# Kernel tuning notes

Measured on AMD Instinct MI355X. Metric: run time of the kernel, lower is better.

The kernel has to match this reference:

```python
import jax, jax.numpy as jnp
import numpy as np
import math

D_MODEL = 512
N_HEADS = 8
MAX_SPAN = 512
SPAN_LOSS_COEF = 2e-4
NEG_INF = -1.0e9
R_SIZE = 4.0


def soft_span_mask(span, max_span, seq_len):
    # span: (H,) clamped span fractions
    i_idx = jnp.arange(seq_len, dtype=span.dtype)[:, None]
    j_idx = jnp.arange(seq_len, dtype=span.dtype)[None, :]
    dist = i_idx - j_idx                                  # (T, T)
    eff_span = (span * max_span)[:, None, None]           # (H, 1, 1)
    x = eff_span - dist[None, :, :]                       # (H, T, T)
    R = jnp.clip((x + 1.0) / R_SIZE, 0.0, 1.0)
    causal_ok = dist[None, :, :] >= 0
    log_R = jnp.maximum(jnp.log(R + 1e-10), NEG_INF)
    return jnp.where(causal_ok & (R > 0), log_R, NEG_INF)  # (H, T, T)


def setup_inputs() -> dict:
    key = jax.random.key(0)
    ks = jax.random.split(key, 6)
    B, T, D = 4, 2048, D_MODEL
    w_scale = 0.02
    return {
        "x": jax.random.normal(ks[0], (B, T, D), dtype=jnp.float32),
        "wq": jax.random.normal(ks[1], (D, D), dtype=jnp.float32) * w_scale,
        "wk": jax.random.normal(ks[2], (D, D), dtype=jnp.float32) * w_scale,
        "wv": jax.random.normal(ks[3], (D, D), dtype=jnp.float32) * w_scale,
        "wo": jax.random.normal(ks[4], (D, D), dtype=jnp.float32) * w_scale,
        "span_params": jax.random.uniform(ks[5], (N_HEADS,), dtype=jnp.float32),
    }


def reference(x, wq, wk, wv, wo, span_params):
    B, T, D = x.shape
    H = N_HEADS
    d_h = D // H

    clamped_span = jnp.clip(span_params, 0.0, 1.0)

    # nn.Linear(bias=False): y = x @ W.T
    Q = (x @ wq.T).reshape(B, T, H, d_h).transpose(0, 2, 1, 3)  # (B,H,T,dh)
    K = (x @ wk.T).reshape(B, T, H, d_h).transpose(0, 2, 1, 3)
    V = (x @ wv.T).reshape(B, T, H, d_h).transpose(0, 2, 1, 3)

    scale = 1.0 / math.sqrt(d_h)
    scores = jnp.einsum("bhqd,bhkd->bhqk", Q, K) * scale        # (B,H,T,T)
    scores = scores + soft_span_mask(clamped_span, MAX_SPAN, T)[None]

    weights = jax.nn.softmax(scores, axis=-1)
    out = jnp.einsum("bhqk,bhkd->bhqd", weights, V)             # (B,H,T,dh)
    out = out.transpose(0, 2, 1, 3).reshape(B, T, D)
    output = out @ wo.T

    span_loss = SPAN_LOSS_COEF * clamped_span.mean()
    return output, span_loss
```

## Files before the change

kernel.cpp:

```cpp
#include <hip/hip_runtime.h>
#include <math.h>

#define T_SEQ   2048
#define DMODEL  512
#define NHEADS  8
#define DH      64
#define NEG_INF -1.0e9f

typedef __attribute__((ext_vector_type(8))) short short8;
typedef __attribute__((ext_vector_type(4))) float f32x4;
typedef unsigned int u32;
typedef unsigned short u16;

__device__ __forceinline__ u16 f2bf(float f) {
    union { float f; u32 u; } w; w.f = f;
    return (u16)((w.u + 0x7fffu + ((w.u >> 16) & 1u)) >> 16);
}

__device__ __forceinline__ void async_load16(const u16* g, u16* l) {
    __builtin_amdgcn_global_load_lds(
        (const __attribute__((address_space(1))) u32*)(const void*)g,
        (__attribute__((address_space(3))) u32*)(void*)l, 16, 0, 0);
}

__global__ void cast_all(const float* __restrict__ x,  const float* __restrict__ wq,
                         const float* __restrict__ wk, const float* __restrict__ wv,
                         const float* __restrict__ wo, const float* __restrict__ sp,
                         u16* __restrict__ xb,  u16* __restrict__ wqb,
                         u16* __restrict__ wkb, u16* __restrict__ wvb,
                         u16* __restrict__ wob, float* __restrict__ loss_out)
{
    const int bid = blockIdx.x;
    const float* src; u16* dst; int i;
    if (bid < 4096) { src = x; dst = xb; i = bid * 256 + threadIdx.x; }
    else {
        const int wsel = (bid - 4096) >> 8;
        src = (wsel == 0) ? wq : (wsel == 1) ? wk : (wsel == 2) ? wv : wo;
        dst = (wsel == 0) ? wqb : (wsel == 1) ? wkb : (wsel == 2) ? wvb : wob;
        i = ((bid - 4096) & 255) * 256 + threadIdx.x;
    }
    float4 v = ((const float4*)src)[i];
    ushort4 o;
    o.x = f2bf(v.x); o.y = f2bf(v.y); o.z = f2bf(v.z); o.w = f2bf(v.w);
    ((ushort4*)dst)[i] = o;
    if (bid == 5119 && threadIdx.x == 0) {
        float s = 0.0f;
        for (int h = 0; h < NHEADS; ++h)
            s += fminf(fmaxf(sp[h], 0.0f), 1.0f);
        loss_out[0] = 2e-4f * (s * 0.125f);
    }
}

__global__ __launch_bounds__(256)
void gemm_bf16(const u16* __restrict__ A,
               const u16* __restrict__ W0, const u16* __restrict__ W1,
               const u16* __restrict__ W2,
               u16* __restrict__ Cb0, u16* __restrict__ Cb1,
               u16* __restrict__ Cb2,
               float* __restrict__ Cf, int scatter)
{
    constexpr int K = 512, BK = 64;
    const u16* W  = (blockIdx.z == 0) ? W0 : (blockIdx.z == 1) ? W1 : W2;
    u16*       Cb = (blockIdx.z == 0) ? Cb0 : (blockIdx.z == 1) ? Cb1 : Cb2;

    __shared__ __align__(16) u16 As[128 * BK];
    __shared__ __align__(16) u16 Bs[128 * BK];

    const int t    = threadIdx.x;
    const int lane = t & 63;
    const int wave = t >> 6;
    const int wm   = wave >> 1, wn = wave & 1;
    const int m0   = blockIdx.x * 128, n0 = blockIdx.y * 128;

    const int srow = t >> 3;
    const int kb   = (t & 7) ^ (srow & 7);
    const u16* gA = A + (size_t)(m0 + srow) * K + kb * 8;
    const u16* gW = W + (size_t)(n0 + srow) * K + kb * 8;

    const int rA = wm * 64 + (lane & 15);
    const int rB = wn * 64 + (lane & 15);
    const int kq = lane >> 4;
    const int offA0 = rA * BK + ((kq      ^ (rA & 7)) * 8);
    const int offA1 = rA * BK + (((4 + kq) ^ (rA & 7)) * 8);
    const int offB0 = rB * BK + ((kq      ^ (rB & 7)) * 8);
    const int offB1 = rB * BK + (((4 + kq) ^ (rB & 7)) * 8);

    f32x4 acc[4][4];
#pragma unroll
    for (int it = 0; it < 4; ++it)
#pragma unroll
        for (int jt = 0; jt < 4; ++jt) acc[it][jt] = (f32x4)0.0f;

    for (int k0 = 0; k0 < K; k0 += BK) {
        __syncthreads();
#pragma unroll
        for (int i = 0; i < 4; ++i) {
            async_load16(gA + k0 + i * (32 * K), As + t * 8 + i * 2048);
            async_load16(gW + k0 + i * (32 * K), Bs + t * 8 + i * 2048);
        }
        __syncthreads();

        short8 af[4][2], bfr[4][2];
#pragma unroll
        for (int it = 0; it < 4; ++it) {
            af[it][0]  = *(const short8*)(As + offA0 + it * 16 * BK);
            af[it][1]  = *(const short8*)(As + offA1 + it * 16 * BK);
            bfr[it][0] = *(const short8*)(Bs + offB0 + it * 16 * BK);
            bfr[it][1] = *(const short8*)(Bs + offB1 + it * 16 * BK);
        }
#pragma unroll
        for (int it = 0; it < 4; ++it)
#pragma unroll
            for (int jt = 0; jt < 4; ++jt) {
                acc[it][jt] = __builtin_amdgcn_mfma_f32_16x16x32_bf16(
                    af[it][0], bfr[jt][0], acc[it][jt], 0, 0, 0);
                acc[it][jt] = __builtin_amdgcn_mfma_f32_16x16x32_bf16(
                    af[it][1], bfr[jt][1], acc[it][jt], 0, 0, 0);
            }
    }

    const int r0 = (lane >> 4) * 4;
    const int cl = lane & 15;
#pragma unroll
    for (int it = 0; it < 4; ++it) {
#pragma unroll
        for (int r = 0; r < 4; ++r) {
            const int row = m0 + wm * 64 + it * 16 + r0 + r;
#pragma unroll
            for (int jt = 0; jt < 4; ++jt) {
                const int col = n0 + wn * 64 + jt * 16 + cl;
                const float v = acc[it][jt][r];
                if (scatter) {
                    const int b = row >> 11, tt = row & 2047;
                    const int h = col >> 6,  d = col & 63;
                    Cb[((size_t)((b * NHEADS + h) * T_SEQ + tt)) * DH + d] = f2bf(v);
                } else {
                    Cf[(size_t)row * DMODEL + col] = v;
                }
            }
        }
    }
}

__global__ __launch_bounds__(256)
void transpose_v(const u16* __restrict__ V, u16* __restrict__ Vt)
{
    __shared__ u16 tile[64][72];
    const int bh = blockIdx.y;
    const int j0 = blockIdx.x * 64;
    const u16* src = V + (size_t)bh * (T_SEQ * DH) + (size_t)j0 * DH;
    u16* dst = Vt + (size_t)bh * (T_SEQ * DH) + j0;
    const int t = threadIdx.x;
    const int jr = t >> 2, c0 = (t & 3) * 16;
    uint4 a = *(const uint4*)(src + (size_t)jr * DH + c0);
    uint4 b = *(const uint4*)(src + (size_t)jr * DH + c0 + 8);
    *(uint4*)&tile[jr][c0]     = a;
    *(uint4*)&tile[jr][c0 + 8] = b;
    __syncthreads();
    const int d = t >> 2, jc = (t & 3) * 16;
    union { uint4 v; u16 s[8]; } pa, pb;
#pragma unroll
    for (int i = 0; i < 8; ++i) pa.s[i] = tile[jc + i][d];
#pragma unroll
    for (int i = 0; i < 8; ++i) pb.s[i] = tile[jc + 8 + i][d];
    *(uint4*)(dst + (size_t)d * T_SEQ + jc)     = pa.v;
    *(uint4*)(dst + (size_t)d * T_SEQ + jc + 8) = pb.v;
}

__global__ __launch_bounds__(256)
void attn_mfma(const u16* __restrict__ Q, const u16* __restrict__ K,
               const u16* __restrict__ Vt, const float* __restrict__ span_params,
               u16* __restrict__ out)
{
    __shared__ __align__(16) u16 Ks[64 * 64];
    __shared__ __align__(16) u16 Vs[64 * 64];
    __shared__ __align__(16) u16 Ps[4][16 * 72];

    const int tid  = threadIdx.x;
    const int lane = tid & 63;
    const int w    = tid >> 6;
    const int nl   = lane & 15;
    const int quad = lane >> 4;
    const int bh   = blockIdx.y;
    const int b    = bh >> 3, h = bh & 7;
    const int i0   = blockIdx.x * 64;
    const int q0   = i0 + w * 16;

    const u16* Qh = Q  + (size_t)bh * (T_SEQ * DH);
    const u16* Kh = K  + (size_t)bh * (T_SEQ * DH);
    const u16* Vh = Vt + (size_t)bh * (DH * T_SEQ);

    float span = span_params[h];
    span = fminf(fmaxf(span, 0.0f), 1.0f);
    const float eff_span = span * 512.0f;
    const int wspan = (int)(eff_span + 1.0f) + 1;

    short8 qf0 = *(const short8*)(Qh + (size_t)(q0 + nl) * DH + quad * 8);
    short8 qf1 = *(const short8*)(Qh + (size_t)(q0 + nl) * DH + 32 + quad * 8);

    const int srow = tid >> 3;
    const int sg   = (tid & 7) ^ (srow & 7);
    const u16* gK = Kh + (size_t)srow * DH + sg * 8;
    const u16* gV = Vh + (size_t)srow * T_SEQ + sg * 8;

    f32x4 o[4];
    float m_r[4], l_r[4];
#pragma unroll
    for (int d = 0; d < 4; ++d) o[d] = (f32x4)0.0f;
#pragma unroll
    for (int r = 0; r < 4; ++r) { m_r[r] = -1.0e30f; l_r[r] = 0.0f; }

    int j_lo = i0 - wspan;
    if (j_lo < 0) j_lo = 0;
    j_lo &= ~63;

    for (int j0 = j_lo; j0 <= i0; j0 += 64) {
        __syncthreads();
        async_load16(gK + (size_t)j0 * DH,            Ks + tid * 8);
        async_load16(gK + (size_t)(j0 + 32) * DH,     Ks + tid * 8 + 2048);
        async_load16(gV + j0,                         Vs + tid * 8);
        async_load16(gV + j0 + (size_t)32 * T_SEQ,    Vs + tid * 8 + 2048);
        __syncthreads();

        f32x4 s[4];
        bool act[4];
#pragma unroll
        for (int n = 0; n < 4; ++n) {
            const int jn = j0 + n * 16;
            act[n] = (jn <= q0 + 15) &&
                     ((float)(q0 - jn - 15) <= eff_span);
            s[n] = (f32x4)0.0f;
            if (act[n]) {
                const int row = n * 16 + nl;
                const u16* kp = Ks + row * 64;
                short8 b0 = *(const short8*)(kp + ((quad ^ (row & 7)) * 8));
                short8 b1 = *(const short8*)(kp + (((4 + quad) ^ (row & 7)) * 8));
                s[n] = __builtin_amdgcn_mfma_f32_16x16x32_bf16(qf0, b0, s[n], 0, 0, 0);
                s[n] = __builtin_amdgcn_mfma_f32_16x16x32_bf16(qf1, b1, s[n], 0, 0, 0);
            }
        }

        float tmax[4] = {-1.0e30f, -1.0e30f, -1.0e30f, -1.0e30f};
#pragma unroll
        for (int n = 0; n < 4; ++n) {
            if (!act[n]) continue;
            const int jn = j0 + n * 16;
            const bool boundary = ((float)(q0 + 15 - jn) > eff_span - 4.0f);
#pragma unroll
            for (int r = 0; r < 4; ++r) {
                const int dist = (q0 + quad * 4 + r) - (jn + nl);
                float sv = NEG_INF;
                if (boundary) {
                    if (dist >= 0) {
                        float xv = eff_span - (float)dist;
                        float R  = fminf(fmaxf((xv + 1.0f) * 0.25f, 0.0f), 1.0f);
                        if (R > 0.0f)
                            sv = s[n][r] * 0.125f +
                                 ((R < 1.0f) ? __logf(R + 1e-10f) : 0.0f);
                    }
                } else {
                    if (dist >= 0) sv = s[n][r] * 0.125f;
                }
                s[n][r] = sv;
                tmax[r] = fmaxf(tmax[r], sv);
            }
        }

        float alpha[4];
#pragma unroll
        for (int r = 0; r < 4; ++r) {
            float t = tmax[r];
            t = fmaxf(t, __shfl_xor(t, 1));
            t = fmaxf(t, __shfl_xor(t, 2));
            t = fmaxf(t, __shfl_xor(t, 4));
            t = fmaxf(t, __shfl_xor(t, 8));
            const float m_new = fmaxf(m_r[r], t);
            alpha[r] = __expf(m_r[r] - m_new);
            m_r[r] = m_new;
        }

        float psum[4] = {0.0f, 0.0f, 0.0f, 0.0f};
#pragma unroll
        for (int n = 0; n < 4; ++n)
#pragma unroll
            for (int r = 0; r < 4; ++r) {
                const float pv = act[n] ? __expf(s[n][r] - m_r[r]) : 0.0f;
                psum[r] += pv;
                Ps[w][(quad * 4 + r) * 72 + n * 16 + nl] = f2bf(pv);
            }
#pragma unroll
        for (int r = 0; r < 4; ++r) {
            float ps = psum[r];
            ps += __shfl_xor(ps, 1);
            ps += __shfl_xor(ps, 2);
            ps += __shfl_xor(ps, 4);
            ps += __shfl_xor(ps, 8);
            l_r[r] = l_r[r] * alpha[r] + ps;
#pragma unroll
            for (int d = 0; d < 4; ++d) o[d][r] *= alpha[r];
        }

        const bool kf0 = act[0] | act[1];
        const bool kf1 = act[2] | act[3];
        const u16* pb = Ps[w] + nl * 72;
        short8 a0 = *(const short8*)(pb + quad * 8);
        short8 a1 = *(const short8*)(pb + 32 + quad * 8);
#pragma unroll
        for (int d = 0; d < 4; ++d) {
            const int vrow = d * 16 + nl;
            const u16* vp = Vs + vrow * 64;
            if (kf0) {
                short8 vb0 = *(const short8*)(vp + ((quad ^ (vrow & 7)) * 8));
                o[d] = __builtin_amdgcn_mfma_f32_16x16x32_bf16(a0, vb0, o[d], 0, 0, 0);
            }
            if (kf1) {
                short8 vb1 = *(const short8*)(vp + (((4 + quad) ^ (vrow & 7)) * 8));
                o[d] = __builtin_amdgcn_mfma_f32_16x16x32_bf16(a1, vb1, o[d], 0, 0, 0);
            }
        }
    }

#pragma unroll
    for (int r = 0; r < 4; ++r) {
        const int qg = q0 + quad * 4 + r;
        const float inv_l = 1.0f / l_r[r];
        u16* op = out + (size_t)(b * T_SEQ + qg) * DMODEL + h * 64;
#pragma unroll
        for (int d = 0; d < 4; ++d)
            op[d * 16 + nl] = f2bf(o[d][r] * inv_l);
    }
}

extern "C" void kernel_launch(void* const* d_in, const int* in_sizes, int n_in,
                              void* d_out, int out_size, void* d_ws, size_t ws_size,
                              hipStream_t stream)
{
    (void)in_sizes; (void)n_in; (void)out_size; (void)ws_size;
    const float* x  = (const float*)d_in[0];
    const float* wq = (const float*)d_in[1];
    const float* wk = (const float*)d_in[2];
    const float* wv = (const float*)d_in[3];
    const float* wo = (const float*)d_in[4];
    const float* sp = (const float*)d_in[5];
    float* out = (float*)d_out;

    const size_t elems = (size_t)4 * T_SEQ * DMODEL;
    u16* xb  = (u16*)d_ws;
    u16* Qb  = xb  + elems;
    u16* Kb  = Qb  + elems;
    u16* Vb  = Kb  + elems;
    u16* Vtb = Vb  + elems;
    u16* Ab  = Vtb + elems;
    u16* wqb = Ab  + elems;
    u16* wkb = wqb + 262144;
    u16* wvb = wkb + 262144;
    u16* wob = wvb + 262144;

    cast_all<<<5120, 256, 0, stream>>>(x, wq, wk, wv, wo, sp,
                                       xb, wqb, wkb, wvb, wob, out + elems);
    gemm_bf16<<<dim3(64, 4, 3), 256, 0, stream>>>(
        xb, wqb, wkb, wvb, Qb, Kb, Vb, nullptr, 1);
    transpose_v<<<dim3(32, 32), 256, 0, stream>>>(Vb, Vtb);
    attn_mfma<<<dim3(32, 32), 256, 0, stream>>>(Qb, Kb, Vtb, sp, Ab);
    gemm_bf16<<<dim3(64, 4, 1), 256, 0, stream>>>(
        Ab, wob, wob, wob, nullptr, nullptr, nullptr, out, 0);
}
```

Before: 165.8 us.

## Halve attention block size, stage QKV scatter through LDS, simplify bf16 rounding

The attention kernel now uses 128-thread blocks covering 32 queries, which doubles the grid and gives finer-grained work under the sliding span window. K/V tile loads are issued in four chunks per thread, and mask handling is split into interior, causal-only and span-boundary paths so fewer tiles pay for the log computation. The QKV GEMM epilogue stages bf16 results in shared memory and writes coalesced 16-byte rows to the per-head layout instead of scattered 2-byte stores. The bf16 conversion switches to round-half-up, which drops ties-to-even and slightly changes numerics. Each attention block now reloads the full 64-key tile for only 32 queries, so K/V reuse drops.

New measurement: 161.0 us. 2.9% less time.

```diff
diff --git a/kernel.cpp b/kernel.cpp
--- a/kernel.cpp
+++ b/kernel.cpp
@@ -14,7 +14,7 @@
 
 __device__ __forceinline__ u16 f2bf(float f) {
     union { float f; u32 u; } w; w.f = f;
-    return (u16)((w.u + 0x7fffu + ((w.u >> 16) & 1u)) >> 16);
+    return (u16)((w.u + 0x8000u) >> 16);
 }
 
 __device__ __forceinline__ void async_load16(const u16* g, u16* l) {
@@ -63,8 +63,9 @@
     const u16* W  = (blockIdx.z == 0) ? W0 : (blockIdx.z == 1) ? W1 : W2;
     u16*       Cb = (blockIdx.z == 0) ? Cb0 : (blockIdx.z == 1) ? Cb1 : Cb2;
 
-    __shared__ __align__(16) u16 As[128 * BK];
-    __shared__ __align__(16) u16 Bs[128 * BK];
+    __shared__ __align__(16) u16 smem[16384];
+    u16* As = smem;
+    u16* Bs = smem + 8192;
 
     const int t    = threadIdx.x;
     const int lane = t & 63;
@@ -121,21 +122,47 @@
 
     const int r0 = (lane >> 4) * 4;
     const int cl = lane & 15;
-#pragma unroll
-    for (int it = 0; it < 4; ++it) {
-#pragma unroll
-        for (int r = 0; r < 4; ++r) {
-            const int row = m0 + wm * 64 + it * 16 + r0 + r;
-#pragma unroll
-            for (int jt = 0; jt < 4; ++jt) {
-                const int col = n0 + wn * 64 + jt * 16 + cl;
-                const float v = acc[it][jt][r];
-                if (scatter) {
-                    const int b = row >> 11, tt = row & 2047;
-                    const int h = col >> 6,  d = col & 63;
-                    Cb[((size_t)((b * NHEADS + h) * T_SEQ + tt)) * DH + d] = f2bf(v);
-                } else {
-                    Cf[(size_t)row * DMODEL + col] = v;
+
+    if (scatter) {
+        constexpr int P = 136;
+#pragma unroll
+        for (int rnd = 0; rnd < 2; ++rnd) {
+            __syncthreads();
+#pragma unroll
+            for (int s = 0; s < 2; ++s) {
+                const int it = rnd * 2 + s;
+                const int lrow = wm * 32 + s * 16 + r0;
+#pragma unroll
+                for (int jt = 0; jt < 4; ++jt) {
+                    const int cc = wn * 64 + jt * 16 + cl;
+#pragma unroll
+                    for (int r = 0; r < 4; ++r)
+                        smem[(lrow + r) * P + cc] = f2bf(acc[it][jt][r]);
+                }
+            }
+            __syncthreads();
+            const int lrow2 = t >> 2;
+            const int h2    = (t >> 1) & 1;
+            const int dhalf = t & 1;
+            const int grow  = m0 + (lrow2 >> 5) * 64 + rnd * 32 + (lrow2 & 31);
+            const int b     = grow >> 11, tt = grow & 2047;
+            const int h     = (n0 >> 6) + h2;
+            u16* dst = Cb + ((size_t)((b * NHEADS + h) * T_SEQ + tt)) * DH + dhalf * 32;
+            const u16* srcl = smem + lrow2 * P + h2 * 64 + dhalf * 32;
+#pragma unroll
+            for (int i = 0; i < 4; ++i)
+                ((uint4*)dst)[i] = *(const uint4*)(srcl + i * 8);
+        }
+    } else {
+#pragma unroll
+        for (int it = 0; it < 4; ++it) {
+#pragma unroll
+            for (int r = 0; r < 4; ++r) {
+                const int row = m0 + wm * 64 + it * 16 + r0 + r;
+#pragma unroll
+                for (int jt = 0; jt < 4; ++jt) {
+                    const int col = n0 + wn * 64 + jt * 16 + cl;
+                    Cf[(size_t)row * DMODEL + col] = acc[it][jt][r];
                 }
             }
         }
@@ -167,14 +194,14 @@
     *(uint4*)(dst + (size_t)d * T_SEQ + jc + 8) = pb.v;
 }
 
-__global__ __launch_bounds__(256)
+__global__ __launch_bounds__(128)
 void attn_mfma(const u16* __restrict__ Q, const u16* __restrict__ K,
                const u16* __restrict__ Vt, const float* __restrict__ span_params,
                u16* __restrict__ out)
 {
     __shared__ __align__(16) u16 Ks[64 * 64];
     __shared__ __align__(16) u16 Vs[64 * 64];
-    __shared__ __align__(16) u16 Ps[4][16 * 72];
+    __shared__ __align__(16) u16 Ps[2][16 * 76];
 
     const int tid  = threadIdx.x;
     const int lane = tid & 63;
@@ -183,7 +210,7 @@
     const int quad = lane >> 4;
     const int bh   = blockIdx.y;
     const int b    = bh >> 3, h = bh & 7;
-    const int i0   = blockIdx.x * 64;
+    const int i0   = blockIdx.x * 32;
     const int q0   = i0 + w * 16;
 
     const u16* Qh = Q  + (size_t)bh * (T_SEQ * DH);
@@ -214,23 +241,24 @@
     if (j_lo < 0) j_lo = 0;
     j_lo &= ~63;
 
-    for (int j0 = j_lo; j0 <= i0; j0 += 64) {
+    for (int j0 = j_lo; j0 <= i0 + 31; j0 += 64) {
         __syncthreads();
-        async_load16(gK + (size_t)j0 * DH,            Ks + tid * 8);
-        async_load16(gK + (size_t)(j0 + 32) * DH,     Ks + tid * 8 + 2048);
-        async_load16(gV + j0,                         Vs + tid * 8);
-        async_load16(gV + j0 + (size_t)32 * T_SEQ,    Vs + tid * 8 + 2048);
+#pragma unroll
+        for (int i = 0; i < 4; ++i) {
+            async_load16(gK + (size_t)(j0 + i * 16) * DH, Ks + tid * 8 + i * 1024);
+            async_load16(gV + j0 + (size_t)(i * 16) * T_SEQ, Vs + tid * 8 + i * 1024);
+        }
         __syncthreads();
 
         f32x4 s[4];
-        bool act[4];
+        bool any[4];
 #pragma unroll
         for (int n = 0; n < 4; ++n) {
             const int jn = j0 + n * 16;
-            act[n] = (jn <= q0 + 15) &&
-                     ((float)(q0 - jn - 15) <= eff_span);
+            any[n] = (jn <= q0 + 15) &&
+                     ((float)(q0 - jn - 15) < eff_span + 1.0f);
             s[n] = (f32x4)0.0f;
-            if (act[n]) {
+            if (any[n]) {
                 const int row = n * 16 + nl;
                 const u16* kp = Ks + row * 64;
                 short8 b0 = *(const short8*)(kp + ((quad ^ (row & 7)) * 8));
@@ -243,14 +271,30 @@
         float tmax[4] = {-1.0e30f, -1.0e30f, -1.0e30f, -1.0e30f};
 #pragma unroll
         for (int n = 0; n < 4; ++n) {
-            if (!act[n]) continue;
+            if (!any[n]) continue;
             const int jn = j0 + n * 16;
-            const bool boundary = ((float)(q0 + 15 - jn) > eff_span - 4.0f);
-#pragma unroll
-            for (int r = 0; r < 4; ++r) {
-                const int dist = (q0 + quad * 4 + r) - (jn + nl);
-                float sv = NEG_INF;
-                if (boundary) {
+            const bool causal_b = (jn + 15 > q0);
+            const bool span_b   = ((float)(q0 + 15 - jn) > eff_span - 3.0f);
+            if (!causal_b && !span_b) {
+#pragma unroll
+                for (int r = 0; r < 4; ++r) {
+                    const float sv = s[n][r] * 0.125f;
+                    s[n][r] = sv;
+                    tmax[r] = fmaxf(tmax[r], sv);
+                }
+            } else if (!span_b) {
+#pragma unroll
+                for (int r = 0; r < 4; ++r) {
+                    const int dist = (q0 + quad * 4 + r) - (jn + nl);
+                    const float sv = (dist >= 0) ? s[n][r] * 0.125f : NEG_INF;
+                    s[n][r] = sv;
+                    tmax[r] = fmaxf(tmax[r], sv);
+                }
+            } else {
+#pragma unroll
+                for (int r = 0; r < 4; ++r) {
+                    const int dist = (q0 + quad * 4 + r) - (jn + nl);
+                    float sv = NEG_INF;
                     if (dist >= 0) {
                         float xv = eff_span - (float)dist;
                         float R  = fminf(fmaxf((xv + 1.0f) * 0.25f, 0.0f), 1.0f);
@@ -258,11 +302,9 @@
                             sv = s[n][r] * 0.125f +
                                  ((R < 1.0f) ? __logf(R + 1e-10f) : 0.0f);
                     }
-                } else {
-                    if (dist >= 0) sv = s[n][r] * 0.125f;
-                }
-                s[n][r] = sv;
-                tmax[r] = fmaxf(tmax[r], sv);
+                    s[n][r] = sv;
+                    tmax[r] = fmaxf(tmax[r], sv);
+                }
             }
         }
 
@@ -281,13 +323,20 @@
 
         float psum[4] = {0.0f, 0.0f, 0.0f, 0.0f};
 #pragma unroll
-        for (int n = 0; n < 4; ++n)
-#pragma unroll
-            for (int r = 0; r < 4; ++r) {
-                const float pv = act[n] ? __expf(s[n][r] - m_r[r]) : 0.0f;
-                psum[r] += pv;
-                Ps[w][(quad * 4 + r) * 72 + n * 16 + nl] = f2bf(pv);
-            }
+        for (int n = 0; n < 4; ++n) {
+            if (any[n]) {
+#pragma unroll
+                for (int r = 0; r < 4; ++r) {
+                    const float pv = __expf(s[n][r] - m_r[r]);
+                    psum[r] += pv;
+                    Ps[w][(quad * 4 + r) * 76 + n * 16 + nl] = f2bf(pv);
+                }
+            } else {
+#pragma unroll
+                for (int r = 0; r < 4; ++r)
+                    Ps[w][(quad * 4 + r) * 76 + n * 16 + nl] = 0;
+            }
+        }
 #pragma unroll
         for (int r = 0; r < 4; ++r) {
             float ps = psum[r];
@@ -300,9 +349,9 @@
             for (int d = 0; d < 4; ++d) o[d][r] *= alpha[r];
         }
 
-        const bool kf0 = act[0] | act[1];
-        const bool kf1 = act[2] | act[3];
-        const u16* pb = Ps[w] + nl * 72;
+        const bool kf0 = any[0] | any[1];
+        const bool kf1 = any[2] | any[3];
+        const u16* pb = Ps[w] + nl * 76;
         short8 a0 = *(const short8*)(pb + quad * 8);
         short8 a1 = *(const short8*)(pb + 32 + quad * 8);
 #pragma unroll
@@ -361,7 +410,7 @@
     gemm_bf16<<<dim3(64, 4, 3), 256, 0, stream>>>(
         xb, wqb, wkb, wvb, Qb, Kb, Vb, nullptr, 1);
     transpose_v<<<dim3(32, 32), 256, 0, stream>>>(Vb, Vtb);
-    attn_mfma<<<dim3(32, 32), 256, 0, stream>>>(Qb, Kb, Vtb, sp, Ab);
+    attn_mfma<<<dim3(64, 32), 128, 0, stream>>>(Qb, Kb, Vtb, sp, Ab);
     gemm_bf16<<<dim3(64, 4, 1), 256, 0, stream>>>(
         Ab, wob, wob, wob, nullptr, nullptr, nullptr, out, 0);
 }
```
